# Optimization experiments

Hardware: AMD Instinct MI355X
Metric: run time of the kernel (lower is better)

## Reference

```python
import jax, jax.numpy as jnp
import numpy as np

NEG_SLOPE = 0.2
N, E, NNZ, IN, H, C = 100000, 50000, 800000, 128, 8, 16


def setup_inputs() -> dict:
    key = jax.random.key(0)
    ks = jax.random.split(key, 8)
    X = jax.random.normal(ks[0], (N, IN), jnp.float32)
    W_typed = jax.random.normal(ks[1], (4, IN, H * C), jnp.float32) * (1.0 / np.sqrt(IN))
    att_e = jax.random.normal(ks[2], (4, H, C), jnp.float32) * 0.1
    att_v = jax.random.normal(ks[3], (4, H, C), jnp.float32) * 0.1
    vertex = jax.random.randint(ks[4], (NNZ,), 0, N, jnp.int32)
    edges = jax.random.randint(ks[5], (NNZ,), 0, E, jnp.int32)
    vtype = jax.random.randint(ks[6], (N,), 0, 4, jnp.int32)
    etype = jax.random.randint(ks[7], (E,), 0, 4, jnp.int32)
    return {"X": X, "W_typed": W_typed, "att_e": att_e, "att_v": att_v,
            "vertex": vertex, "edges": edges, "vtype": vtype, "etype": etype}


def _segment_softmax(logits, seg, num):
    # numerically-stable softmax over segments (PyG-style, eps in denominator)
    m = jax.ops.segment_max(logits, seg, num_segments=num)
    ex = jnp.exp(logits - m[seg])
    s = jax.ops.segment_sum(ex, seg, num_segments=num)
    return ex / (s[seg] + 1e-16)


def reference(X, W_typed, att_e, att_v, vertex, edges, vtype, etype):
    # typed linear: project with all 4 type weights, select per node type
    Xall = jnp.einsum('ni,tio->tno', X, W_typed)        # [4, N, H*C]
    X0 = Xall[vtype, jnp.arange(N)]                     # [N, H*C]
    Xn = X0.reshape(N, H, C)
    Xve = Xn[vertex]                                    # [NNZ, H, C] gather vertex->incidence
    # vertex->edge attention, typed by edge type of each incidence
    beta = jnp.sum(Xve * att_e[etype[edges]], axis=-1)  # [NNZ, H]
    beta = jax.nn.leaky_relu(beta, NEG_SLOPE)
    beta = _segment_softmax(beta, edges, E)
    Xe = jax.nn.relu(jax.ops.segment_sum(Xve * beta[..., None], edges, num_segments=E))  # [E, H, C]
    Xe = Xe[edges]                                      # [NNZ, H, C] gather edge->incidence
    # edge->vertex attention, typed by node type of each incidence's vertex
    alpha = jnp.sum(Xe * att_v[vtype[vertex]], axis=-1)  # [NNZ, H]
    alpha = jax.nn.leaky_relu(alpha, NEG_SLOPE)
    alpha = _segment_softmax(alpha, vertex, N)
    Xv = jax.ops.segment_sum(Xe * alpha[..., None], vertex, num_segments=N)  # [N, H, C]
    return Xv.reshape(N, H * C)
```

## Files before the change

kernel.cpp:

```cpp
#include <hip/hip_runtime.h>

typedef __attribute__((ext_vector_type(8))) short bf16x8;
typedef __attribute__((ext_vector_type(4))) float f32x4;

#define NEG_SLOPE 0.2f

__device__ __forceinline__ unsigned short f2bf(float f){
  unsigned u = __float_as_uint(f);
  u = (u + 0x7fffu + ((u >> 16) & 1u)) >> 16;
  return (unsigned short)u;
}
__device__ __forceinline__ float bflo(unsigned u){ return __uint_as_float(u << 16); }
__device__ __forceinline__ float bfhi(unsigned u){ return __uint_as_float(u & 0xffff0000u); }

__global__ __launch_bounds__(256) void k_histprep(
    const int* __restrict__ edges, const int* __restrict__ vertex, int NNZ,
    int* __restrict__ cnt, int E, int nbHist,
    const float* __restrict__ W, short* __restrict__ Bfrag){
  if ((int)blockIdx.x < nbHist){
    int i = blockIdx.x * 256 + threadIdx.x;
    if (i < NNZ){
      atomicAdd(cnt + edges[i], 1);
      atomicAdd(cnt + E + vertex[i], 1);
    }
    return;
  }
  int u = ((int)blockIdx.x - nbHist) * 256 + threadIdx.x;
  int j = u & 7, lane = (u >> 3) & 63, ct = (u >> 9) & 31, ks = u >> 14;
  int k = ks * 32 + ((lane >> 4) << 3) + j;
  int col = (ct << 4) + (lane & 15);
  int t = col >> 7, o = col & 127;
  Bfrag[u] = (short)f2bf(W[(t * 128 + k) * 128 + o]);
}

__global__ __launch_bounds__(256) void k_scanA(const int* __restrict__ cnt, int S,
                                               int* __restrict__ bsum){
  __shared__ int sh[256];
  int base = blockIdx.x * 1024 + threadIdx.x * 4;
  int s = 0;
  #pragma unroll
  for (int k = 0; k < 4; ++k){ int idx = base + k; if (idx < S) s += cnt[idx]; }
  sh[threadIdx.x] = s; __syncthreads();
  for (int off = 128; off > 0; off >>= 1){
    if (threadIdx.x < off) sh[threadIdx.x] += sh[threadIdx.x + off];
    __syncthreads();
  }
  if (threadIdx.x == 0) bsum[blockIdx.x] = sh[0];
}

__global__ void k_scanB(int* bsum, int nb){
  if (threadIdx.x == 0 && blockIdx.x == 0){
    int run = 0;
    for (int b = 0; b < nb; ++b){ int v = bsum[b]; bsum[b] = run; run += v; }
  }
}

__global__ __launch_bounds__(256) void k_scanC(const int* __restrict__ cnt, int S,
    const int* __restrict__ bsum, int* __restrict__ offs, int* __restrict__ cursor){
  __shared__ int sh[256];
  int t = threadIdx.x;
  int base = blockIdx.x * 1024 + t * 4;
  int c[4]; int s = 0;
  #pragma unroll
  for (int k = 0; k < 4; ++k){ int idx = base + k; c[k] = (idx < S) ? cnt[idx] : 0; s += c[k]; }
  sh[t] = s; __syncthreads();
  for (int off = 1; off < 256; off <<= 1){
    int v = (t >= off) ? sh[t - off] : 0; __syncthreads();
    sh[t] += v; __syncthreads();
  }
  int run = bsum[blockIdx.x] + sh[t] - s;
  #pragma unroll
  for (int k = 0; k < 4; ++k){
    int idx = base + k;
    if (idx < S){ offs[idx] = run; cursor[idx] = run; run += c[k]; }
  }
}

__global__ __launch_bounds__(256, 2) void k_gemm_place(const float* __restrict__ X,
    const int* __restrict__ vtype, const short* __restrict__ Bfrag,
    unsigned short* __restrict__ X0, int N, int nbGemm,
    const int* __restrict__ edges, const int* __restrict__ vertex, int NNZ,
    int* __restrict__ cursor, int* __restrict__ rows, int nbPlace){
  __shared__ short shB[32 * 64 * 8];
  const int tid = threadIdx.x;
  const int q = (int)blockIdx.x / 3, r = (int)blockIdx.x % 3;

  if (r != 0){
    int hb = 2 * q + (r - 1);
    if (hb < nbPlace){
      int i = hb * 256 + tid;
      if (i < NNZ){
        int pos = atomicAdd(cursor + edges[i], 1);
        rows[pos] = vertex[i];
      }
    }
    return;
  }
  if (q >= nbGemm) return;

  const int w = tid >> 6, lane = tid & 63;
  const int blockRow = q * 64;
  const int m = lane & 15, qq = lane >> 4;
  const int node = blockRow + w * 16 + m;

  bf16x8 afrag[4];
  #pragma unroll
  for (int ks = 0; ks < 4; ++ks){
    bf16x8 f;
    if (node < N){
      const float4* src = (const float4*)(X + (size_t)node * 128 + ks * 32 + qq * 8);
      float4 a = src[0], b = src[1];
      f[0]=(short)f2bf(a.x); f[1]=(short)f2bf(a.y); f[2]=(short)f2bf(a.z); f[3]=(short)f2bf(a.w);
      f[4]=(short)f2bf(b.x); f[5]=(short)f2bf(b.y); f[6]=(short)f2bf(b.z); f[7]=(short)f2bf(b.w);
    } else {
      #pragma unroll
      for (int z = 0; z < 8; ++z) f[z] = 0;
    }
    afrag[ks] = f;
  }

  f32x4 acc[32];
  #pragma unroll
  for (int ct = 0; ct < 32; ++ct){
    acc[ct][0]=0.f; acc[ct][1]=0.f; acc[ct][2]=0.f; acc[ct][3]=0.f;
  }

  for (int ks = 0; ks < 4; ++ks){
    __syncthreads();
    const bf16x8* src = (const bf16x8*)(Bfrag + (((size_t)ks * 32 + w * 8) * 64 + lane) * 8);
    bf16x8* dst = (bf16x8*)(shB + ((w * 8) * 64 + lane) * 8);
    #pragma unroll
    for (int ci = 0; ci < 8; ++ci) dst[ci * 64] = src[ci * 64];
    __syncthreads();
    bf16x8 af = afrag[ks];
    #pragma unroll
    for (int ct = 0; ct < 32; ++ct){
      bf16x8 bf = *(const bf16x8*)(shB + (ct * 64 + lane) * 8);
      acc[ct] = __builtin_amdgcn_mfma_f32_16x16x32_bf16(af, bf, acc[ct], 0, 0, 0);
    }
  }

  const int col0 = lane & 15;
  #pragma unroll
  for (int rr = 0; rr < 4; ++rr){
    int noder = blockRow + w * 16 + qq * 4 + rr;
    if (noder >= N) continue;
    int tt = vtype[noder];
    #pragma unroll
    for (int ct = 0; ct < 32; ++ct){
      if ((ct >> 3) == tt)
        X0[(size_t)noder * 128 + (ct & 7) * 16 + col0] = f2bf(acc[ct][rr]);
    }
  }
}

template<int OUT_BF16, int DO_RELU>
__device__ __forceinline__ void seg_body(const unsigned* __restrict__ feat,
    const float* __restrict__ att, const int* __restrict__ rows_sorted,
    const int* __restrict__ offs, const int* __restrict__ cnt,
    const int* __restrict__ stype, void* __restrict__ outbuf,
    int S, int blockId, int tid){
  int wid = tid >> 6, lane = tid & 63;
  int s = blockId * 4 + wid;
  if (s >= S) return;
  int t = stype[s];
  float a0 = att[t * 128 + 2 * lane], a1 = att[t * 128 + 2 * lane + 1];
  int start = offs[s], len = cnt[s];
  float denom = 0.f, acc0 = 0.f, acc1 = 0.f;

  for (int base = 0; base < len; base += 64){
    int m = len - base; if (m > 64) m = 64;
    int idx = 0;
    if (lane < m) idx = rows_sorted[start + base + lane];

    unsigned u0 = 0, u1 = 0, u2 = 0, u3 = 0;
    {
      int r;
      r = __shfl(idx, 0); if (0 < m) u0 = feat[(size_t)r * 64 + lane];
      r = __shfl(idx, 1); if (1 < m) u1 = feat[(size_t)r * 64 + lane];
      r = __shfl(idx, 2); if (2 < m) u2 = feat[(size_t)r * 64 + lane];
      r = __shfl(idx, 3); if (3 < m) u3 = feat[(size_t)r * 64 + lane];
    }
    for (int j = 0; j < m; j += 2){
      unsigned ua = u0, ub = u1;
      u0 = u2; u1 = u3;
      if (j + 4 < m){ int rn = __shfl(idx, j + 4); u2 = feat[(size_t)rn * 64 + lane]; }
      if (j + 5 < m){ int rn = __shfl(idx, j + 5); u3 = feat[(size_t)rn * 64 + lane]; }

      float xa0 = bflo(ua), xa1 = bfhi(ua);
      float xb0 = bflo(ub), xb1 = bfhi(ub);
      float pa = xa0 * a0 + xa1 * a1;
      float pb = xb0 * a0 + xb1 * a1;
      pa += __shfl_xor(pa, 1);  pb += __shfl_xor(pb, 1);
      pa += __shfl_xor(pa, 2);  pb += __shfl_xor(pb, 2);
      pa += __shfl_xor(pa, 4);  pb += __shfl_xor(pb, 4);
      pa = pa > 0.f ? pa : NEG_SLOPE * pa;
      float wa = __expf(pa);
      denom += wa; acc0 += wa * xa0; acc1 += wa * xa1;
      if (j + 1 < m){
        pb = pb > 0.f ? pb : NEG_SLOPE * pb;
        float wb = __expf(pb);
        denom += wb; acc0 += wb * xb0; acc1 += wb * xb1;
      }
    }
  }
  float inv = 1.f / (denom + 1e-16f);
  float v0 = acc0 * inv, v1 = acc1 * inv;
  if (DO_RELU){ v0 = fmaxf(v0, 0.f); v1 = fmaxf(v1, 0.f); }
  if (OUT_BF16){
    unsigned pw = (unsigned)f2bf(v0) | ((unsigned)f2bf(v1) << 16);
    ((unsigned*)outbuf)[(size_t)s * 64 + lane] = pw;
  } else {
    ((float2*)outbuf)[(size_t)s * 64 + lane] = make_float2(v0, v1);
  }
}

__global__ __launch_bounds__(256) void k_place_seg1(
    const int* __restrict__ edges, const int* __restrict__ vertex, int NNZ,
    int* __restrict__ cursor, int* __restrict__ rows, int E,
    int nbPlace, int nbSeg,
    const unsigned* __restrict__ X0, const float* __restrict__ att_e,
    const int* __restrict__ offs, const int* __restrict__ cnt,
    const int* __restrict__ etype, void* __restrict__ Xe){
  const int q = (int)blockIdx.x / 5, r = (int)blockIdx.x % 5;
  if (r == 0){
    if (q < nbPlace){
      int i = q * 256 + threadIdx.x;
      if (i < NNZ){
        int pos = atomicAdd(cursor + E + vertex[i], 1);
        rows[pos] = edges[i];
      }
    }
    return;
  }
  int segBlk = q * 4 + (r - 1);
  if (segBlk >= nbSeg) return;
  seg_body<1, 1>(X0, att_e, rows, offs, cnt, etype, Xe, E, segBlk, threadIdx.x);
}

__global__ __launch_bounds__(256) void k_seg2(const unsigned* __restrict__ Xe,
    const float* __restrict__ att_v, const int* __restrict__ rows,
    const int* __restrict__ offs, const int* __restrict__ cnt,
    const int* __restrict__ vtype, float* __restrict__ out, int N){
  seg_body<0, 0>(Xe, att_v, rows, offs, cnt, vtype, out, N,
                 (int)blockIdx.x, threadIdx.x);
}

extern "C" void kernel_launch(void* const* d_in, const int* in_sizes, int n_in,
                              void* d_out, int out_size, void* d_ws, size_t ws_size,
                              hipStream_t stream){
  const float* X      = (const float*)d_in[0];
  const float* W      = (const float*)d_in[1];
  const float* att_e  = (const float*)d_in[2];
  const float* att_v  = (const float*)d_in[3];
  const int*   vertex = (const int*)d_in[4];
  const int*   edges  = (const int*)d_in[5];
  const int*   vtype  = (const int*)d_in[6];
  const int*   etype  = (const int*)d_in[7];
  float* out = (float*)d_out;
  const int N   = in_sizes[0] / 128;
  const int NNZ = in_sizes[4];
  const int E   = in_sizes[7];
  const int S   = E + N;

  char* wp = (char*)d_ws;
  int* cnt    = (int*)wp; wp += (size_t)S * 4;
  int* offs   = (int*)wp; wp += (size_t)S * 4;
  int* cursor = (int*)wp; wp += (size_t)S * 4;
  int* bsum   = (int*)wp; wp += 1024;
  int* rows   = (int*)wp; wp += (size_t)2 * NNZ * 4;
  unsigned short* X0 = (unsigned short*)wp; wp += (size_t)N * 128 * 2;
  unsigned short* Xe = (unsigned short*)wp; wp += (size_t)E * 128 * 2;
  short* Bfrag = (short*)wp; wp += (size_t)65536 * 2;

  hipMemsetAsync(cnt, 0, (size_t)S * 4, stream);

  const int nbI = (NNZ + 255) / 256;
  const int nbG = (N + 63) / 64;
  const int nbS = (S + 1023) / 1024;
  const int nbSeg1 = (E + 3) / 4;

  k_histprep<<<nbI + 256, 256, 0, stream>>>(edges, vertex, NNZ, cnt, E, nbI,
                                            W, Bfrag);

  k_scanA<<<nbS, 256, 0, stream>>>(cnt, S, bsum);
  k_scanB<<<1, 64, 0, stream>>>(bsum, nbS);
  k_scanC<<<nbS, 256, 0, stream>>>(cnt, S, bsum, offs, cursor);

  k_gemm_place<<<3 * nbG, 256, 0, stream>>>(X, vtype, Bfrag,
      (unsigned short*)X0, N, nbG, edges, vertex, NNZ, cursor, rows, nbI);

  k_place_seg1<<<5 * nbI, 256, 0, stream>>>(edges, vertex, NNZ, cursor,
      rows, E, nbI, nbSeg1, (const unsigned*)X0, att_e, offs, cnt, etype, Xe);

  k_seg2<<<(N + 3) / 4, 256, 0, stream>>>((const unsigned*)Xe, att_v,
      rows, offs + E, cnt + E, vtype, out, N);
}
```

Baseline: 367.7 us.

## Bucket nodes by type so the typed GEMM computes only the matching weight slice

Nodes are counted by type, and a counting sort builds a padded index list of node ids grouped by type, with each type bucket aligned to 64 rows. Each GEMM block now handles 64 nodes of a single type, loads only that type's 128-column weight slice into shared memory, and issues 8 MFMA column tiles instead of 32. This removes the 4x redundant projection and shrinks the accumulator and LDS footprint, which allows 3 blocks per CU. The cost is extra histogram and scatter passes, an extra memset, indirect row gathers of X, and scattered writes to X0.

```diff
diff --git a/kernel.cpp b/kernel.cpp
--- a/kernel.cpp
+++ b/kernel.cpp
@@ -16,16 +16,25 @@
 __global__ __launch_bounds__(256) void k_histprep(
     const int* __restrict__ edges, const int* __restrict__ vertex, int NNZ,
     int* __restrict__ cnt, int E, int nbHist,
+    const int* __restrict__ vtype, int N, int* __restrict__ tcnt, int nbHN,
     const float* __restrict__ W, short* __restrict__ Bfrag){
-  if ((int)blockIdx.x < nbHist){
-    int i = blockIdx.x * 256 + threadIdx.x;
+  int b = (int)blockIdx.x;
+  if (b < nbHist){
+    int i = b * 256 + threadIdx.x;
     if (i < NNZ){
       atomicAdd(cnt + edges[i], 1);
       atomicAdd(cnt + E + vertex[i], 1);
     }
     return;
   }
-  int u = ((int)blockIdx.x - nbHist) * 256 + threadIdx.x;
+  b -= nbHist;
+  if (b < nbHN){
+    int i = b * 256 + threadIdx.x;
+    if (i < N) atomicAdd(tcnt + vtype[i], 1);
+    return;
+  }
+  b -= nbHN;
+  int u = b * 256 + threadIdx.x;
   int j = u & 7, lane = (u >> 3) & 63, ct = (u >> 9) & 31, ks = u >> 14;
   int k = ks * 32 + ((lane >> 4) << 3) + j;
   int col = (ct << 4) + (lane & 15);
@@ -48,18 +57,43 @@
   if (threadIdx.x == 0) bsum[blockIdx.x] = sh[0];
 }
 
-__global__ void k_scanB(int* bsum, int nb){
+__global__ void k_scanB(int* bsum, int nb, const int* __restrict__ tcnt,
+                        int* __restrict__ pbase){
   if (threadIdx.x == 0 && blockIdx.x == 0){
     int run = 0;
     for (int b = 0; b < nb; ++b){ int v = bsum[b]; bsum[b] = run; run += v; }
+    int pb = 0;
+    for (int t = 0; t < 4; ++t){
+      pbase[t] = pb;
+      pb += ((tcnt[t] + 63) >> 6) << 6;
+    }
+    pbase[4] = pb;
   }
 }
 
 __global__ __launch_bounds__(256) void k_scanC(const int* __restrict__ cnt, int S,
-    const int* __restrict__ bsum, int* __restrict__ offs, int* __restrict__ cursor){
+    const int* __restrict__ bsum, int* __restrict__ offs, int* __restrict__ cursor,
+    int nbS, const int* __restrict__ vtype, int N, const int* __restrict__ pbase,
+    int* __restrict__ tcur, int* __restrict__ nsorted){
   __shared__ int sh[256];
+  __shared__ int gbase[4];
   int t = threadIdx.x;
-  int base = blockIdx.x * 1024 + t * 4;
+  int b = (int)blockIdx.x;
+  if (b >= nbS){
+    int* lcnt = sh;
+    if (t < 4) lcnt[t] = 0;
+    __syncthreads();
+    int i = (b - nbS) * 256 + t;
+    int tt = 0, rank = 0;
+    bool valid = i < N;
+    if (valid){ tt = vtype[i]; rank = atomicAdd(&lcnt[tt], 1); }
+    __syncthreads();
+    if (t < 4 && lcnt[t] > 0) gbase[t] = atomicAdd(tcur + t, lcnt[t]);
+    __syncthreads();
+    if (valid) nsorted[pbase[tt] + gbase[tt] + rank] = i;
+    return;
+  }
+  int base = b * 1024 + t * 4;
   int c[4]; int s = 0;
   #pragma unroll
   for (int k = 0; k < 4; ++k){ int idx = base + k; c[k] = (idx < S) ? cnt[idx] : 0; s += c[k]; }
@@ -68,7 +102,7 @@
     int v = (t >= off) ? sh[t - off] : 0; __syncthreads();
     sh[t] += v; __syncthreads();
   }
-  int run = bsum[blockIdx.x] + sh[t] - s;
+  int run = bsum[b] + sh[t] - s;
   #pragma unroll
   for (int k = 0; k < 4; ++k){
     int idx = base + k;
@@ -76,12 +110,12 @@
   }
 }
 
-__global__ __launch_bounds__(256, 2) void k_gemm_place(const float* __restrict__ X,
-    const int* __restrict__ vtype, const short* __restrict__ Bfrag,
-    unsigned short* __restrict__ X0, int N, int nbGemm,
+__global__ __launch_bounds__(256, 3) void k_gemm_place(const float* __restrict__ X,
+    const short* __restrict__ Bfrag, const int* __restrict__ nsorted,
+    const int* __restrict__ pbase, unsigned short* __restrict__ X0,
     const int* __restrict__ edges, const int* __restrict__ vertex, int NNZ,
     int* __restrict__ cursor, int* __restrict__ rows, int nbPlace){
-  __shared__ short shB[32 * 64 * 8];
+  __shared__ short shB[8 * 4 * 64 * 8];
   const int tid = threadIdx.x;
   const int q = (int)blockIdx.x / 3, r = (int)blockIdx.x % 3;
 
@@ -96,18 +130,29 @@
     }
     return;
   }
-  if (q >= nbGemm) return;
+
+  const int rowIdx = q * 64;
+  const int t = (rowIdx >= pbase[1]) + (rowIdx >= pbase[2]) + (rowIdx >= pbase[3]);
+
+  const bf16x8* Bv = (const bf16x8*)Bfrag;
+  bf16x8* shBv = (bf16x8*)shB;
+  #pragma unroll
+  for (int v = 0; v < 8; ++v){
+    int item = v * 256 + tid;
+    int slab = item >> 6, ln = item & 63;
+    int ks = slab >> 3, ctl = slab & 7;
+    shBv[item] = Bv[((ks * 32 + 8 * t + ctl) * 64) + ln];
+  }
 
   const int w = tid >> 6, lane = tid & 63;
-  const int blockRow = q * 64;
   const int m = lane & 15, qq = lane >> 4;
-  const int node = blockRow + w * 16 + m;
+  const int node = nsorted[rowIdx + w * 16 + m];
 
   bf16x8 afrag[4];
   #pragma unroll
   for (int ks = 0; ks < 4; ++ks){
     bf16x8 f;
-    if (node < N){
+    if (node >= 0){
       const float4* src = (const float4*)(X + (size_t)node * 128 + ks * 32 + qq * 8);
       float4 a = src[0], b = src[1];
       f[0]=(short)f2bf(a.x); f[1]=(short)f2bf(a.y); f[2]=(short)f2bf(a.z); f[3]=(short)f2bf(a.w);
@@ -119,38 +164,30 @@
     afrag[ks] = f;
   }
 
-  f32x4 acc[32];
-  #pragma unroll
-  for (int ct = 0; ct < 32; ++ct){
+  f32x4 acc[8];
+  #pragma unroll
+  for (int ct = 0; ct < 8; ++ct){
     acc[ct][0]=0.f; acc[ct][1]=0.f; acc[ct][2]=0.f; acc[ct][3]=0.f;
   }
 
-  for (int ks = 0; ks < 4; ++ks){
-    __syncthreads();
-    const bf16x8* src = (const bf16x8*)(Bfrag + (((size_t)ks * 32 + w * 8) * 64 + lane) * 8);
-    bf16x8* dst = (bf16x8*)(shB + ((w * 8) * 64 + lane) * 8);
+  __syncthreads();
+  #pragma unroll
+  for (int ctl = 0; ctl < 8; ++ctl){
     #pragma unroll
-    for (int ci = 0; ci < 8; ++ci) dst[ci * 64] = src[ci * 64];
-    __syncthreads();
-    bf16x8 af = afrag[ks];
+    for (int ks = 0; ks < 4; ++ks){
+      bf16x8 bf = shBv[(ks * 8 + ctl) * 64 + lane];
+      acc[ctl] = __builtin_amdgcn_mfma_f32_16x16x32_bf16(afrag[ks], bf, acc[ctl], 0, 0, 0);
+    }
+  }
+
+  const int col0 = lane & 15;
+  #pragma unroll
+  for (int rr = 0; rr < 4; ++rr){
+    int row = nsorted[rowIdx + w * 16 + qq * 4 + rr];
+    if (row < 0) continue;
     #pragma unroll
-    for (int ct = 0; ct < 32; ++ct){
-      bf16x8 bf = *(const bf16x8*)(shB + (ct * 64 + lane) * 8);
-      acc[ct] = __builtin_amdgcn_mfma_f32_16x16x32_bf16(af, bf, acc[ct], 0, 0, 0);
-    }
-  }
-
-  const int col0 = lane & 15;
-  #pragma unroll
-  for (int rr = 0; rr < 4; ++rr){
-    int noder = blockRow + w * 16 + qq * 4 + rr;
-    if (noder >= N) continue;
-    int tt = vtype[noder];
-    #pragma unroll
-    for (int ct = 0; ct < 32; ++ct){
-      if ((ct >> 3) == tt)
-        X0[(size_t)noder * 128 + (ct & 7) * 16 + col0] = f2bf(acc[ct][rr]);
-    }
+    for (int ctl = 0; ctl < 8; ++ctl)
+      X0[(size_t)row * 128 + ctl * 16 + col0] = f2bf(acc[ctl][rr]);
   }
 }
 
@@ -263,32 +300,40 @@
   const int E   = in_sizes[7];
   const int S   = E + N;
 
+  const int nbI = (NNZ + 255) / 256;
+  const int nbHN = (N + 255) / 256;
+  const int nbS = (S + 1023) / 1024;
+  const int nbSeg1 = (E + 3) / 4;
+  const int nbPad = (N + 252 + 63) / 64;
+  const int nsortedCap = nbPad * 64;
+
   char* wp = (char*)d_ws;
   int* cnt    = (int*)wp; wp += (size_t)S * 4;
+  int* tcnt   = (int*)wp; wp += 16;
+  int* tcur   = (int*)wp; wp += 16;
   int* offs   = (int*)wp; wp += (size_t)S * 4;
   int* cursor = (int*)wp; wp += (size_t)S * 4;
   int* bsum   = (int*)wp; wp += 1024;
+  int* pbase  = (int*)wp; wp += 32;
   int* rows   = (int*)wp; wp += (size_t)2 * NNZ * 4;
+  int* nsorted= (int*)wp; wp += (size_t)nsortedCap * 4;
   unsigned short* X0 = (unsigned short*)wp; wp += (size_t)N * 128 * 2;
   unsigned short* Xe = (unsigned short*)wp; wp += (size_t)E * 128 * 2;
   short* Bfrag = (short*)wp; wp += (size_t)65536 * 2;
 
-  hipMemsetAsync(cnt, 0, (size_t)S * 4, stream);
-
-  const int nbI = (NNZ + 255) / 256;
-  const int nbG = (N + 63) / 64;
-  const int nbS = (S + 1023) / 1024;
-  const int nbSeg1 = (E + 3) / 4;
-
-  k_histprep<<<nbI + 256, 256, 0, stream>>>(edges, vertex, NNZ, cnt, E, nbI,
-                                            W, Bfrag);
+  hipMemsetAsync(cnt, 0, (size_t)(S + 8) * 4, stream);
+  hipMemsetAsync(nsorted, 0xFF, (size_t)nsortedCap * 4, stream);
+
+  k_histprep<<<nbI + nbHN + 256, 256, 0, stream>>>(edges, vertex, NNZ, cnt, E,
+      nbI, vtype, N, tcnt, nbHN, W, Bfrag);
 
   k_scanA<<<nbS, 256, 0, stream>>>(cnt, S, bsum);
-  k_scanB<<<1, 64, 0, stream>>>(bsum, nbS);
-  k_scanC<<<nbS, 256, 0, stream>>>(cnt, S, bsum, offs, cursor);
-
-  k_gemm_place<<<3 * nbG, 256, 0, stream>>>(X, vtype, Bfrag,
-      (unsigned short*)X0, N, nbG, edges, vertex, NNZ, cursor, rows, nbI);
+  k_scanB<<<1, 64, 0, stream>>>(bsum, nbS, tcnt, pbase);
+  k_scanC<<<nbS + nbHN, 256, 0, stream>>>(cnt, S, bsum, offs, cursor,
+      nbS, vtype, N, pbase, tcur, nsorted);
+
+  k_gemm_place<<<3 * nbPad, 256, 0, stream>>>(X, Bfrag, nsorted, pbase,
+      (unsigned short*)X0, edges, vertex, NNZ, cursor, rows, nbI);
 
   k_place_seg1<<<5 * nbI, 256, 0, stream>>>(edges, vertex, NNZ, cursor,
       rows, E, nbI, nbSeg1, (const unsigned*)X0, att_e, offs, cnt, etype, Xe);
```

Measured after the change: 885.0 us. 141% more time.
